# Kernel optimization log

Measured on AMD Instinct MI355X. Metric: run time of the kernel, lower is better.

The kernel has to match this reference:

```python
import jax, jax.numpy as jnp
import numpy as np

NEG = -9e15  # matches torch's -9000000000000000.0 mask value
LN_EPS = 1e-5


def gat_layer(x, adj, W, a, gamma, beta):
    # x: [M, N, Fin], adj: [M, N, N]
    h = x @ W                                  # [M, N, H]
    H = W.shape[1]
    # a([h_i, h_j]) decomposes: e_ij = leakyrelu(h_i.a1 + h_j.a2)
    s_i = h @ a[:H]                            # [M, N]
    s_j = h @ a[H:]                            # [M, N]
    e = jax.nn.leaky_relu(s_i[:, :, None] + s_j[:, None, :], 0.2)
    e = jnp.where(adj > 0, e, NEG)
    att = jax.nn.softmax(e, axis=2)
    hp = jnp.einsum('mij,mjh->mih', att, h)    # bmm aggregation
    mu = hp.mean(-1, keepdims=True)
    var = hp.var(-1, keepdims=True)
    hn = (hp - mu) * jax.lax.rsqrt(var + LN_EPS) * gamma + beta
    return jax.nn.elu(hn)


def lstm_dir(x_seq, Wih, Whh, bih, bhh):
    # x_seq: [B, T, D]; Wih: [D, 4H]; Whh: [H, 4H]; gate order i,f,g,o (torch)
    B = x_seq.shape[0]
    H = Whh.shape[0]
    xg = jnp.einsum('btd,dk->btk', x_seq, Wih) + bih + bhh  # precompute input gates

    def step(carry, xg_t):
        h, c = carry
        g = xg_t + h @ Whh
        i, f, gg, o = jnp.split(g, 4, axis=-1)
        c = jax.nn.sigmoid(f) * c + jax.nn.sigmoid(i) * jnp.tanh(gg)
        h = jax.nn.sigmoid(o) * jnp.tanh(c)
        return (h, c), h

    init = (jnp.zeros((B, H), x_seq.dtype), jnp.zeros((B, H), x_seq.dtype))
    (h_last, _), hs = jax.lax.scan(step, init, jnp.swapaxes(xg, 0, 1))
    return jnp.swapaxes(hs, 0, 1), h_last


def bilstm_layer(x_seq, Wih, Whh, bih, bhh):
    of, hf = lstm_dir(x_seq, Wih[0], Whh[0], bih[0], bhh[0])
    ob, hb = lstm_dir(x_seq[:, ::-1], Wih[1], Whh[1], bih[1], bhh[1])
    return jnp.concatenate([of, ob[:, ::-1]], axis=-1), hf, hb


def setup_inputs() -> dict:
    key = jax.random.key(0)
    ks = jax.random.split(key, 20)
    B, S, N, F, H = 4, 64, 256, 32, 64

    def rn(k, shape, fan_in):
        return jax.random.normal(k, shape, jnp.float32) / np.float32(np.sqrt(fan_in))

    return {
        'x': jax.random.normal(ks[0], (B, S, N, F), jnp.float32),
        'adj': jax.random.randint(ks[1], (B, S, N, N), 0, 2).astype(jnp.float32),
        'gat0_W': rn(ks[2], (F, H), F),
        'gat0_a': rn(ks[3], (2 * H,), 2 * H),
        'gat0_g': jnp.ones((H,), jnp.float32),
        'gat0_b': jnp.zeros((H,), jnp.float32),
        'gat1_W': rn(ks[4], (H, H), H),
        'gat1_a': rn(ks[5], (2 * H,), 2 * H),
        'gat1_g': jnp.ones((H,), jnp.float32),
        'gat1_b': jnp.zeros((H,), jnp.float32),
        'res_W': rn(ks[6], (F, H), F),
        'res_b': jnp.zeros((H,), jnp.float32),
        'alpha_gate': jnp.asarray(0.01, jnp.float32),
        'l0_Wih': rn(ks[7], (2, H, 4 * H), H),
        'l0_Whh': rn(ks[8], (2, H, 4 * H), H),
        'l0_bih': rn(ks[9], (2, 4 * H), H),
        'l0_bhh': rn(ks[10], (2, 4 * H), H),
        'l1_Wih': rn(ks[11], (2, 2 * H, 4 * H), 2 * H),
        'l1_Whh': rn(ks[12], (2, H, 4 * H), H),
        'l1_bih': rn(ks[13], (2, 4 * H), H),
        'l1_bhh': rn(ks[14], (2, 4 * H), H),
        'fc_W': rn(ks[15], (2 * H, 1), 2 * H),
        'fc_b': jnp.zeros((1,), jnp.float32),
    }


def reference(x, adj, gat0_W, gat0_a, gat0_g, gat0_b, gat1_W, gat1_a, gat1_g, gat1_b,
              res_W, res_b, alpha_gate, l0_Wih, l0_Whh, l0_bih, l0_bhh,
              l1_Wih, l1_Whh, l1_bih, l1_bhh, fc_W, fc_b):
    B, S, N, F = x.shape
    x_flat = x.reshape(B * S, N, F)
    adj_flat = adj.reshape(B * S, N, N)

    g = gat_layer(x_flat, adj_flat, gat0_W, gat0_a, gat0_g, gat0_b)
    g = gat_layer(g, adj_flat, gat1_W, gat1_a, gat1_g, gat1_b)

    res = x_flat @ res_W + res_b
    gate = jnp.clip(alpha_gate, 0.0, 1.0)
    comb = res + gate * g                       # [B*S, N, H]
    Hd = comb.shape[-1]

    # [B,S,N,H] -> [B,N,S,H] -> [B*N, S, H]
    seq = comb.reshape(B, S, N, Hd).transpose(0, 2, 1, 3).reshape(B * N, S, Hd)

    o1, _, _ = bilstm_layer(seq, l0_Wih, l0_Whh, l0_bih, l0_bhh)
    _, hf, hb = bilstm_layer(o1, l1_Wih, l1_Whh, l1_bih, l1_bhh)

    final = jnp.concatenate([hf, hb], axis=-1)  # h_n[-2], h_n[-1]
    pred = final @ fc_W + fc_b
    return pred.reshape(B, N, 1)
```

## Files before the change

### kernel.cpp

```cpp
#include <hip/hip_runtime.h>
#include <math.h>

#define BB 4
#define SS 64
#define NN 256
#define FF 32
#define HH 64
#define MM (BB*SS)
#define NSEQ (BB*NN)
#define TT SS
#define MROWS (NSEQ*TT)

__device__ __forceinline__ float fast_rcp(float x) { return __builtin_amdgcn_rcpf(x); }
__device__ __forceinline__ float sigmoid_f(float x) { return fast_rcp(1.0f + __expf(-x)); }
__device__ __forceinline__ float tanh_f(float x) {
    float t = __expf(-2.0f * fabsf(x));
    float r = (1.0f - t) * fast_rcp(1.0f + t);
    return copysignf(r, x);
}

__device__ __forceinline__ void lds_barrier() {
    asm volatile("s_waitcnt lgkmcnt(0)" ::: "memory");
    __builtin_amdgcn_s_barrier();
    __builtin_amdgcn_sched_barrier(0);
}

typedef __bf16 bf16x8 __attribute__((ext_vector_type(8)));
typedef float  f32x4  __attribute__((ext_vector_type(4)));

__device__ __forceinline__ __bf16 bfh(float x) {
    unsigned u = __float_as_uint(x);
    unsigned r = (u + 0x7FFFu + ((u >> 16) & 1u)) >> 16;
    return __builtin_bit_cast(__bf16, (unsigned short)r);
}
__device__ __forceinline__ float bf2f(__bf16 b) {
    unsigned u = ((unsigned)__builtin_bit_cast(unsigned short, b)) << 16;
    return __uint_as_float(u);
}

template<int FIN>
__global__ __launch_bounds__(256) void gat_kernel(
    const float* __restrict__ xin,
    const float* __restrict__ adj,
    const float* __restrict__ W,
    const float* __restrict__ a,
    const float* __restrict__ gamma_, const float* __restrict__ beta_,
    float* __restrict__ gout)
{
    __shared__ __align__(16) float u_f32[256 * 68];
    __shared__ __align__(16) __bf16 p_hi[256 * 40];
    __shared__ __align__(16) __bf16 p_lo[256 * 40];
    __shared__ float s1s[256], s2s[256], srow[256];

    __bf16* F_hi = (__bf16*)u_f32;
    __bf16* F_lo = F_hi + 64 * 264;

    const int m    = blockIdx.x;
    const int tid  = threadIdx.x;
    const int lane = tid & 63;
    const int wv   = tid >> 6;
    const int nl   = lane & 15;
    const int lq   = lane >> 4;

    {
        const int c = tid & 63;
        const int w = tid >> 6;
        float wreg[FIN];
#pragma unroll
        for (int f = 0; f < FIN; ++f) wreg[f] = W[f * 64 + c];
        const float* xm = xin + (size_t)m * NN * FIN;
        for (int i0 = 0; i0 < 64; ++i0) {
            int i = (i0 << 2) | w;
            float acc = 0.0f;
#pragma unroll
            for (int f4 = 0; f4 < FIN / 4; ++f4) {
                float4 xv = *(const float4*)&xm[i * FIN + f4 * 4];
                acc += xv.x * wreg[f4*4] + xv.y * wreg[f4*4+1]
                     + xv.z * wreg[f4*4+2] + xv.w * wreg[f4*4+3];
            }
            u_f32[i * 68 + c] = acc;
        }
    }
    __syncthreads();

    float hr[64];
    {
        const float* hp = &u_f32[tid * 68];
        float acc1 = 0.0f, acc2 = 0.0f;
#pragma unroll
        for (int c4 = 0; c4 < 16; ++c4) {
            float4 hv = *(const float4*)&hp[c4 * 4];
            hr[c4*4+0] = hv.x; hr[c4*4+1] = hv.y; hr[c4*4+2] = hv.z; hr[c4*4+3] = hv.w;
            float4 av1 = *(const float4*)&a[c4 * 4];
            float4 av2 = *(const float4*)&a[64 + c4 * 4];
            acc1 += hv.x * av1.x + hv.y * av1.y + hv.z * av1.z + hv.w * av1.w;
            acc2 += hv.x * av2.x + hv.y * av2.y + hv.z * av2.z + hv.w * av2.w;
        }
        s1s[tid] = acc1; s2s[tid] = acc2;
    }
    __syncthreads();
    {
#pragma unroll
        for (int c = 0; c < 64; ++c) {
            __bf16 hh = bfh(hr[c]);
            F_hi[c * 264 + tid] = hh;
            F_lo[c * 264 + tid] = bfh(hr[c] - bf2f(hh));
        }
    }

    const float* adjr = adj + ((size_t)m * NN + tid) * NN;
    const float s1v = s1s[tid];
    float srow_acc = 0.0f;

    f32x4 acc[4][4];
#pragma unroll
    for (int mt = 0; mt < 4; ++mt)
#pragma unroll
        for (int nt = 0; nt < 4; ++nt)
            acc[mt][nt] = (f32x4){0.0f, 0.0f, 0.0f, 0.0f};

    float4 adjreg[8];
#pragma unroll
    for (int q = 0; q < 8; ++q) adjreg[q] = *(const float4*)&adjr[q * 4];

    for (int ch = 0; ch < 8; ++ch) {
        {
            float pv[32];
#pragma unroll
            for (int q = 0; q < 8; ++q) {
                float4 av = adjreg[q];
                float4 sv = *(const float4*)&s2s[ch * 32 + q * 4];
                float e0 = s1v + sv.x, e1 = s1v + sv.y, e2 = s1v + sv.z, e3 = s1v + sv.w;
                e0 = (e0 > 0.0f) ? e0 : 0.2f * e0;
                e1 = (e1 > 0.0f) ? e1 : 0.2f * e1;
                e2 = (e2 > 0.0f) ? e2 : 0.2f * e2;
                e3 = (e3 > 0.0f) ? e3 : 0.2f * e3;
                float p0 = (av.x > 0.0f) ? __expf(e0) : 0.0f;
                float p1 = (av.y > 0.0f) ? __expf(e1) : 0.0f;
                float p2 = (av.z > 0.0f) ? __expf(e2) : 0.0f;
                float p3 = (av.w > 0.0f) ? __expf(e3) : 0.0f;
                srow_acc += (p0 + p1) + (p2 + p3);
                pv[q*4+0] = p0; pv[q*4+1] = p1; pv[q*4+2] = p2; pv[q*4+3] = p3;
            }
#pragma unroll
            for (int b = 0; b < 4; ++b) {
                bf16x8 h8, l8;
#pragma unroll
                for (int j = 0; j < 8; ++j) {
                    __bf16 hh = bfh(pv[b*8+j]);
                    h8[j] = hh;
                    l8[j] = bfh(pv[b*8+j] - bf2f(hh));
                }
                *(bf16x8*)&p_hi[tid * 40 + b * 8] = h8;
                *(bf16x8*)&p_lo[tid * 40 + b * 8] = l8;
            }
        }
        if (ch < 7) {
#pragma unroll
            for (int q = 0; q < 8; ++q)
                adjreg[q] = *(const float4*)&adjr[(ch + 1) * 32 + q * 4];
        }
        lds_barrier();

        bf16x8 pah[4], pal[4], fbh[4], fbl[4];
#pragma unroll
        for (int mt = 0; mt < 4; ++mt) {
            int row = wv * 64 + mt * 16 + nl;
            pah[mt] = *(const bf16x8*)&p_hi[row * 40 + lq * 8];
            pal[mt] = *(const bf16x8*)&p_lo[row * 40 + lq * 8];
        }
#pragma unroll
        for (int nt = 0; nt < 4; ++nt) {
            int fo = (nt * 16 + nl) * 264 + ch * 32 + lq * 8;
            fbh[nt] = *(const bf16x8*)&F_hi[fo];
            fbl[nt] = *(const bf16x8*)&F_lo[fo];
        }
#pragma unroll
        for (int mt = 0; mt < 4; ++mt)
#pragma unroll
            for (int nt = 0; nt < 4; ++nt)
                acc[mt][nt] = __builtin_amdgcn_mfma_f32_16x16x32_bf16(
                    pah[mt], fbh[nt], acc[mt][nt], 0, 0, 0);
#pragma unroll
        for (int mt = 0; mt < 4; ++mt)
#pragma unroll
            for (int nt = 0; nt < 4; ++nt)
                acc[mt][nt] = __builtin_amdgcn_mfma_f32_16x16x32_bf16(
                    pal[mt], fbh[nt], acc[mt][nt], 0, 0, 0);
#pragma unroll
        for (int mt = 0; mt < 4; ++mt)
#pragma unroll
            for (int nt = 0; nt < 4; ++nt)
                acc[mt][nt] = __builtin_amdgcn_mfma_f32_16x16x32_bf16(
                    pah[mt], fbl[nt], acc[mt][nt], 0, 0, 0);

        lds_barrier();
    }

    srow[tid] = srow_acc;
    __syncthreads();

    float gm[4], bt[4];
#pragma unroll
    for (int nt = 0; nt < 4; ++nt) {
        gm[nt] = gamma_[nt * 16 + nl];
        bt[nt] = beta_[nt * 16 + nl];
    }
#pragma unroll
    for (int mt = 0; mt < 4; ++mt) {
#pragma unroll
        for (int r = 0; r < 4; ++r) {
            int row = wv * 64 + mt * 16 + lq * 4 + r;
            float rinv = fast_rcp(srow[row]);
            float v[4];
            float sm = 0.0f, sq = 0.0f;
#pragma unroll
            for (int nt = 0; nt < 4; ++nt) {
                v[nt] = acc[mt][nt][r] * rinv;
                sm += v[nt]; sq += v[nt] * v[nt];
            }
#pragma unroll
            for (int off = 1; off < 16; off <<= 1) {
                sm += __shfl_xor(sm, off);
                sq += __shfl_xor(sq, off);
            }
            float mu  = sm * (1.0f / 64.0f);
            float var = sq * (1.0f / 64.0f) - mu * mu;
            float rs  = rsqrtf(var + 1e-5f);
            float* gp = &gout[((size_t)m * NN + row) * 64];
#pragma unroll
            for (int nt = 0; nt < 4; ++nt) {
                float hn = (v[nt] - mu) * rs * gm[nt] + bt[nt];
                gp[nt * 16 + nl] = (hn > 0.0f) ? hn : (__expf(hn) - 1.0f);
            }
        }
    }
}

__global__ __launch_bounds__(256) void combine_kernel(
    const float* __restrict__ x,
    const float* __restrict__ g1,
    const float* __restrict__ res_W,
    const float* __restrict__ res_b,
    const float* __restrict__ alpha_p,
    float* __restrict__ seqout)
{
    int row = blockIdx.x * 4 + (threadIdx.x >> 6);
    int h = threadIdx.x & 63;
    int mg = row >> 8, n = row & 255;
    int b = mg >> 6, s = mg & 63;
    const float* xr = x + (size_t)row * 32;
    float acc = res_b[h];
#pragma unroll
    for (int f4 = 0; f4 < 8; ++f4) {
        float4 xv = *(const float4*)&xr[f4 * 4];
        acc += xv.x * res_W[(f4*4    ) * 64 + h] + xv.y * res_W[(f4*4 + 1) * 64 + h]
             + xv.z * res_W[(f4*4 + 2) * 64 + h] + xv.w * res_W[(f4*4 + 3) * 64 + h];
    }
    float alpha = fminf(fmaxf(alpha_p[0], 0.0f), 1.0f);
    acc += alpha * g1[(size_t)row * 64 + h];
    seqout[(((size_t)(b * NN + n)) * TT + s) * 64 + h] = acc;
}

template<int K>
__global__ __launch_bounds__(256) void wcvt_kernel(
    const float* __restrict__ Wih, __bf16* __restrict__ Wh, __bf16* __restrict__ Wl)
{
    constexpr int NKC = K / 32;
    int idx = blockIdx.x * 256 + threadIdx.x;
    int j   = idx & 7;
    int nl  = (idx >> 3) & 15;
    int g   = (idx >> 7) & 3;
    int ng  = (idx >> 9) & 15;
    int rest = idx >> 13;
    int kc  = rest & (NKC - 1);
    int dir = rest / NKC;
    int k = kc * 32 + g * 8 + j;
    int n = ng * 16 + nl;
    float x = Wih[((size_t)dir * K + k) * 256 + n];
    __bf16 h = bfh(x);
    Wh[idx] = h;
    Wl[idx] = bfh(x - bf2f(h));
}

__global__ __launch_bounds__(256) void whhcvt_kernel(
    const float* __restrict__ W0, const float* __restrict__ W1,
    __bf16* __restrict__ outw)
{
    int idx = blockIdx.x * 256 + threadIdx.x;
    int lay = idx >> 15;
    int r   = idx & 32767;
    int j   = r & 7;
    int nl  = (r >> 3) & 15;
    int g   = (r >> 7) & 3;
    int ng  = (r >> 9) & 15;
    int rest = r >> 13;
    int kc  = rest & 1;
    int dir = rest >> 1;
    int k = kc * 32 + g * 8 + j;
    int n = ng * 16 + nl;
    const float* W = lay ? W1 : W0;
    float x = W[((size_t)dir * 64 + k) * 256 + n];
    __bf16 h = bfh(x);
    outw[lay * 65536 + r]         = h;
    outw[lay * 65536 + 32768 + r] = bfh(x - bf2f(h));
}

template<int K>
__global__ __launch_bounds__(256, 2) void xg_mfma_kernel(
    const float* __restrict__ A,
    const __bf16* __restrict__ Wh,
    const __bf16* __restrict__ Wl,
    const float* __restrict__ bih,
    const float* __restrict__ bhh,
    float* __restrict__ xg)
{
    constexpr int NKC = K / 32;
    __shared__ __bf16 a_h[2][128 * 32];
    __shared__ __bf16 a_l[2][128 * 32];

    const int tid  = threadIdx.x;
    const int lane = tid & 63;
    const int w    = tid >> 6;
    const int wr   = w >> 1, wc = w & 1;

    int bid = blockIdx.x;
    int wg  = (bid >> 3) | ((bid & 7) << 8);
    int cd  = wg & 3;
    int m0  = (wg >> 2) * 128;
    int dir = cd >> 1;
    const int kq = (cd & 1) * 2 + wc;

    f32x4 acc[4][4];
#pragma unroll
    for (int mi = 0; mi < 4; ++mi)
#pragma unroll
        for (int ni = 0; ni < 4; ++ni)
            acc[mi][ni] = (f32x4){0.0f, 0.0f, 0.0f, 0.0f};

    const int srow = tid >> 1;
    const int g0   = (tid & 1) * 2;
    const float* abase = A + (size_t)(m0 + srow) * K + (tid & 1) * 16;
    const int soff0 = srow * 32 + (( g0      ^ (srow & 3)) * 8);
    const int soff1 = srow * 32 + (((g0 + 1) ^ (srow & 3)) * 8);

    int aoff[4];
#pragma unroll
    for (int mi = 0; mi < 4; ++mi)
        aoff[mi] = (wr * 64 + mi * 16 + (lane & 15)) * 32
                 + (((lane >> 4) ^ (lane & 3)) * 8);

    auto cvtstore = [&](const float* f, int buf) {
        bf16x8 h0, h1, l0, l1;
#pragma unroll
        for (int i = 0; i < 8; ++i) {
            __bf16 ha = bfh(f[i]);
            __bf16 hb = bfh(f[8 + i]);
            h0[i] = ha; l0[i] = bfh(f[i]     - bf2f(ha));
            h1[i] = hb; l1[i] = bfh(f[8 + i] - bf2f(hb));
        }
        *(bf16x8*)&a_h[buf][soff0] = h0;
        *(bf16x8*)&a_h[buf][soff1] = h1;
        *(bf16x8*)&a_l[buf][soff0] = l0;
        *(bf16x8*)&a_l[buf][soff1] = l1;
    };

    {
        float f[16];
#pragma unroll
        for (int i = 0; i < 4; ++i) {
            float4 v = *(const float4*)(abase + i * 4);
            f[i*4+0] = v.x; f[i*4+1] = v.y; f[i*4+2] = v.z; f[i*4+3] = v.w;
        }
        cvtstore(f, 0);
    }
    lds_barrier();

    int buf = 0;
    for (int kc = 0; kc < NKC; ++kc) {
        float f[16];
        if (kc + 1 < NKC) {
#pragma unroll
            for (int i = 0; i < 4; ++i) {
                float4 v = *(const float4*)(abase + (kc + 1) * 32 + i * 4);
                f[i*4+0] = v.x; f[i*4+1] = v.y; f[i*4+2] = v.z; f[i*4+3] = v.w;
            }
        }
        bf16x8 bh[4], bl[4];
#pragma unroll
        for (int ni = 0; ni < 4; ++ni) {
            size_t fb = ((size_t)((dir * NKC + kc) * 16 + ni * 4 + kq)) * 512 + lane * 8;
            bh[ni] = *(const bf16x8*)(Wh + fb);
            bl[ni] = *(const bf16x8*)(Wl + fb);
        }
        bf16x8 ah[4], al[4];
#pragma unroll
        for (int mi = 0; mi < 4; ++mi) {
            ah[mi] = *(const bf16x8*)&a_h[buf][aoff[mi]];
            al[mi] = *(const bf16x8*)&a_l[buf][aoff[mi]];
        }
#pragma unroll
        for (int mi = 0; mi < 4; ++mi)
#pragma unroll
            for (int ni = 0; ni < 4; ++ni)
                acc[mi][ni] = __builtin_amdgcn_mfma_f32_16x16x32_bf16(
                    ah[mi], bh[ni], acc[mi][ni], 0, 0, 0);
#pragma unroll
        for (int mi = 0; mi < 4; ++mi)
#pragma unroll
            for (int ni = 0; ni < 4; ++ni)
                acc[mi][ni] = __builtin_amdgcn_mfma_f32_16x16x32_bf16(
                    al[mi], bh[ni], acc[mi][ni], 0, 0, 0);
#pragma unroll
        for (int mi = 0; mi < 4; ++mi)
#pragma unroll
            for (int ni = 0; ni < 4; ++ni)
                acc[mi][ni] = __builtin_amdgcn_mfma_f32_16x16x32_bf16(
                    ah[mi], bl[ni], acc[mi][ni], 0, 0, 0);

        if (kc + 1 < NKC) cvtstore(f, buf ^ 1);
        lds_barrier();
        buf ^= 1;
    }

    const int kcol = kq * 16 + (lane & 15);
    float bias4[4];
#pragma unroll
    for (int g = 0; g < 4; ++g)
        bias4[g] = bih[dir * 256 + g * 64 + kcol] + bhh[dir * 256 + g * 64 + kcol];
#pragma unroll
    for (int mi = 0; mi < 4; ++mi) {
        int mrow = m0 + wr * 64 + mi * 16 + ((lane >> 4) << 2);
#pragma unroll
        for (int r = 0; r < 4; ++r) {
            float4 v = make_float4(acc[mi][0][r] + bias4[0], acc[mi][1][r] + bias4[1],
                                   acc[mi][2][r] + bias4[2], acc[mi][3][r] + bias4[3]);
            *(float4*)&xg[((size_t)dir * MROWS + mrow + r) * 256 + kcol * 4] = v;
        }
    }
}

__global__ __launch_bounds__(256, 2) void lstm_rec_kernel(
    const float* __restrict__ xg,
    const __bf16* __restrict__ whhf,
    float* __restrict__ out,
    int write_all)
{
    const int tid  = threadIdx.x;
    const int wv   = tid >> 6;
    const int lane = tid & 63;
    const int nl   = lane & 15;
    const int lq   = lane >> 4;

    const int bid  = blockIdx.x;
    const int dir  = bid & 1;
    const int seq0 = (bid >> 1) * 4;

    const __bf16* wh = whhf;
    const __bf16* wl = whhf + 32768;
    bf16x8 bh[2][4], bl[2][4];
#pragma unroll
    for (int kc = 0; kc < 2; ++kc)
#pragma unroll
        for (int g = 0; g < 4; ++g) {
            size_t fb = ((size_t)((dir * 2 + kc) * 16 + g * 4 + wv)) * 512 + lane * 8;
            bh[kc][g] = *(const bf16x8*)(wh + fb);
            bl[kc][g] = *(const bf16x8*)(wl + fb);
        }

    __shared__ __align__(16) __bf16 h_hi[2048];
    __shared__ __align__(16) __bf16 h_lo[2048];
    {
        uint4 z = {0, 0, 0, 0};
        *(uint4*)&h_hi[tid * 8] = z;
        *(uint4*)&h_lo[tid * 8] = z;
    }

    const int k   = wv * 16 + nl;
    const int g8k = k >> 3;

    float c = 0.0f;
    float4 xa = {}, xb = {};

    const float* pxg = xg + (((size_t)dir * NSEQ + seq0 + lq) * TT
                             + (dir ? (TT - 1) : 0)) * 256 + k * 4;
    const int dstep = dir ? -256 : 256;
    float* pout = out + (((size_t)(seq0 + lq)) * TT + (dir ? (TT - 1) : 0)) * 128
                + dir * 64 + k;
    const int ostep = dir ? -128 : 128;

    auto load_xg = [&](float4& d) {
        d = *(const float4*)pxg;
        pxg += dstep;
    };

    int buf = 0;
    auto step_body = [&](int step, float4& xcur, float4& xnext, bool pre) {
        const int aof0 = buf * 1024 + nl * 64 + (((0 + lq) ^ (nl & 7)) * 8);
        const int aof1 = buf * 1024 + nl * 64 + (((4 + lq) ^ (nl & 7)) * 8);
        bf16x8 ah0 = *(const bf16x8*)&h_hi[aof0];
        bf16x8 ah1 = *(const bf16x8*)&h_hi[aof1];
        bf16x8 al0 = *(const bf16x8*)&h_lo[aof0];
        bf16x8 al1 = *(const bf16x8*)&h_lo[aof1];

        if (pre) load_xg(xnext);

        f32x4 acc[4];
#pragma unroll
        for (int g = 0; g < 4; ++g) acc[g] = (f32x4){0.0f, 0.0f, 0.0f, 0.0f};
#pragma unroll
        for (int g = 0; g < 4; ++g)
            acc[g] = __builtin_amdgcn_mfma_f32_16x16x32_bf16(ah0, bh[0][g], acc[g], 0, 0, 0);
#pragma unroll
        for (int g = 0; g < 4; ++g)
            acc[g] = __builtin_amdgcn_mfma_f32_16x16x32_bf16(ah1, bh[1][g], acc[g], 0, 0, 0);
#pragma unroll
        for (int g = 0; g < 4; ++g)
            acc[g] = __builtin_amdgcn_mfma_f32_16x16x32_bf16(al0, bh[0][g], acc[g], 0, 0, 0);
#pragma unroll
        for (int g = 0; g < 4; ++g)
            acc[g] = __builtin_amdgcn_mfma_f32_16x16x32_bf16(al1, bh[1][g], acc[g], 0, 0, 0);
#pragma unroll
        for (int g = 0; g < 4; ++g)
            acc[g] = __builtin_amdgcn_mfma_f32_16x16x32_bf16(ah0, bl[0][g], acc[g], 0, 0, 0);
#pragma unroll
        for (int g = 0; g < 4; ++g)
            acc[g] = __builtin_amdgcn_mfma_f32_16x16x32_bf16(ah1, bl[1][g], acc[g], 0, 0, 0);

        float pre4[4];
#pragma unroll
        for (int g = 0; g < 4; ++g) {
            float b0 = __shfl(acc[g][0], nl);
            float b1 = __shfl(acc[g][1], nl);
            float b2 = __shfl(acc[g][2], nl);
            float b3 = __shfl(acc[g][3], nl);
            float v01 = (lq & 1) ? b1 : b0;
            float v23 = (lq & 1) ? b3 : b2;
            pre4[g] = (lq & 2) ? v23 : v01;
        }

        float iv = sigmoid_f(pre4[0] + xcur.x);
        float fv = sigmoid_f(pre4[1] + xcur.y);
        float gv = tanh_f  (pre4[2] + xcur.z);
        float ov = sigmoid_f(pre4[3] + xcur.w);
        c = fv * c + iv * gv;
        float h = ov * tanh_f(c);
        int off = (buf ^ 1) * 1024 + lq * 64 + ((g8k ^ lq) * 8) + (k & 7);
        __bf16 hh = bfh(h);
        h_hi[off] = hh;
        h_lo[off] = bfh(h - bf2f(hh));
        if (write_all)
            pout[0] = h;
        else if (step == TT - 1)
            out[(size_t)(seq0 + lq) * 128 + dir * 64 + k] = h;
        pout += ostep;
        lds_barrier();
        buf ^= 1;
    };

    load_xg(xa);
    lds_barrier();

    for (int step = 0; step < TT; step += 2) {
        step_body(step,     xa, xb, true);
        step_body(step + 1, xb, xa, step + 2 < TT);
    }
}

__global__ __launch_bounds__(256) void fc_kernel(
    const float* __restrict__ fin,
    const float* __restrict__ fc_W,
    const float* __restrict__ fc_b,
    float* __restrict__ outp)
{
    int s = blockIdx.x * 256 + threadIdx.x;
    const float* fr = fin + (size_t)s * 128;
    float acc = fc_b[0];
#pragma unroll
    for (int k4 = 0; k4 < 32; ++k4) {
        float4 fv = *(const float4*)&fr[k4 * 4];
        float4 wv2 = *(const float4*)&fc_W[k4 * 4];
        acc += fv.x * wv2.x + fv.y * wv2.y + fv.z * wv2.z + fv.w * wv2.w;
    }
    outp[s] = acc;
}

extern "C" void kernel_launch(void* const* d_in, const int* in_sizes, int n_in,
                              void* d_out, int out_size, void* d_ws, size_t ws_size,
                              hipStream_t stream) {
    const float* x       = (const float*)d_in[0];
    const float* adj     = (const float*)d_in[1];
    const float* gat0_W  = (const float*)d_in[2];
    const float* gat0_a  = (const float*)d_in[3];
    const float* gat0_g  = (const float*)d_in[4];
    const float* gat0_b  = (const float*)d_in[5];
    const float* gat1_W  = (const float*)d_in[6];
    const float* gat1_a  = (const float*)d_in[7];
    const float* gat1_g  = (const float*)d_in[8];
    const float* gat1_b  = (const float*)d_in[9];
    const float* res_W   = (const float*)d_in[10];
    const float* res_b   = (const float*)d_in[11];
    const float* alpha_g = (const float*)d_in[12];
    const float* l0_Wih  = (const float*)d_in[13];
    const float* l0_Whh  = (const float*)d_in[14];
    const float* l0_bih  = (const float*)d_in[15];
    const float* l0_bhh  = (const float*)d_in[16];
    const float* l1_Wih  = (const float*)d_in[17];
    const float* l1_Whh  = (const float*)d_in[18];
    const float* l1_bih  = (const float*)d_in[19];
    const float* l1_bhh  = (const float*)d_in[20];
    const float* fc_W    = (const float*)d_in[21];
    const float* fc_b    = (const float*)d_in[22];

    float* ws = (float*)d_ws;
    float* g0    = ws;
    float* g1    = ws + 4194304;
    float* seq   = ws + 8388608;
    float* xg    = ws + 12582912;
    float* fin   = ws + 46137344;
    float* o1    = ws;

    __bf16* w0h = (__bf16*)(ws + 46137344);
    __bf16* w0l = w0h + 2 * 64 * 256;
    __bf16* w1h = w0l + 2 * 64 * 256;
    __bf16* w1l = w1h + 2 * 128 * 256;

    __bf16* whhf = (__bf16*)seq;

    wcvt_kernel<64><<<128, 256, 0, stream>>>(l0_Wih, w0h, w0l);
    wcvt_kernel<128><<<256, 256, 0, stream>>>(l1_Wih, w1h, w1l);
    gat_kernel<32><<<MM, 256, 0, stream>>>(x, adj, gat0_W, gat0_a, gat0_g, gat0_b, g0);
    gat_kernel<64><<<MM, 256, 0, stream>>>(g0, adj, gat1_W, gat1_a, gat1_g, gat1_b, g1);
    combine_kernel<<<(BB*SS*NN)/4, 256, 0, stream>>>(x, g1, res_W, res_b, alpha_g, seq);
    xg_mfma_kernel<64><<<2048, 256, 0, stream>>>(seq, w0h, w0l, l0_bih, l0_bhh, xg);
    whhcvt_kernel<<<256, 256, 0, stream>>>(l0_Whh, l1_Whh, whhf);
    lstm_rec_kernel<<<512, 256, 0, stream>>>(xg, whhf, o1, 1);
    xg_mfma_kernel<128><<<2048, 256, 0, stream>>>(o1, w1h, w1l, l1_bih, l1_bhh, xg);
    lstm_rec_kernel<<<512, 256, 0, stream>>>(xg, whhf + 65536, fin, 0);
    fc_kernel<<<NSEQ/256, 256, 0, stream>>>(fin, fc_W, fc_b, (float*)d_out);
}
```

Measured before the change: 470.6 us.

## Use 512 threads per GAT block, splitting each node row across two threads

The GAT kernel now runs 512 threads per block. Each node row is handled by a pair of threads that split the feature columns and adjacency columns, with shuffle reductions for the attention scores and row sums. Each wave now covers 32 rows instead of 64 in the MFMA aggregation. The aim is to hide more latency with more waves and to lower per-thread register pressure (hr, adjreg, acc). In exchange there are extra shuffles and barriers that span more waves.

```diff
diff --git a/kernel.cpp b/kernel.cpp
--- a/kernel.cpp
+++ b/kernel.cpp
@@ -39,7 +39,7 @@
 }
 
 template<int FIN>
-__global__ __launch_bounds__(256) void gat_kernel(
+__global__ __launch_bounds__(512) void gat_kernel(
     const float* __restrict__ xin,
     const float* __restrict__ adj,
     const float* __restrict__ W,
@@ -61,16 +61,17 @@
     const int wv   = tid >> 6;
     const int nl   = lane & 15;
     const int lq   = lane >> 4;
+    const int row2 = tid >> 1;
+    const int half = tid & 1;
 
     {
         const int c = tid & 63;
-        const int w = tid >> 6;
         float wreg[FIN];
 #pragma unroll
         for (int f = 0; f < FIN; ++f) wreg[f] = W[f * 64 + c];
         const float* xm = xin + (size_t)m * NN * FIN;
-        for (int i0 = 0; i0 < 64; ++i0) {
-            int i = (i0 << 2) | w;
+        for (int i0 = 0; i0 < 32; ++i0) {
+            int i = (i0 << 3) | wv;
             float acc = 0.0f;
 #pragma unroll
             for (int f4 = 0; f4 < FIN / 4; ++f4) {
@@ -83,53 +84,56 @@
     }
     __syncthreads();
 
-    float hr[64];
+    float hr[32];
     {
-        const float* hp = &u_f32[tid * 68];
+        const float* hp = &u_f32[row2 * 68 + half * 32];
         float acc1 = 0.0f, acc2 = 0.0f;
 #pragma unroll
-        for (int c4 = 0; c4 < 16; ++c4) {
+        for (int c4 = 0; c4 < 8; ++c4) {
             float4 hv = *(const float4*)&hp[c4 * 4];
             hr[c4*4+0] = hv.x; hr[c4*4+1] = hv.y; hr[c4*4+2] = hv.z; hr[c4*4+3] = hv.w;
-            float4 av1 = *(const float4*)&a[c4 * 4];
-            float4 av2 = *(const float4*)&a[64 + c4 * 4];
+            float4 av1 = *(const float4*)&a[half * 32 + c4 * 4];
+            float4 av2 = *(const float4*)&a[64 + half * 32 + c4 * 4];
             acc1 += hv.x * av1.x + hv.y * av1.y + hv.z * av1.z + hv.w * av1.w;
             acc2 += hv.x * av2.x + hv.y * av2.y + hv.z * av2.z + hv.w * av2.w;
         }
-        s1s[tid] = acc1; s2s[tid] = acc2;
+        acc1 += __shfl_xor(acc1, 1);
+        acc2 += __shfl_xor(acc2, 1);
+        if (half == 0) { s1s[row2] = acc1; s2s[row2] = acc2; }
     }
     __syncthreads();
     {
 #pragma unroll
-        for (int c = 0; c < 64; ++c) {
-            __bf16 hh = bfh(hr[c]);
-            F_hi[c * 264 + tid] = hh;
-            F_lo[c * 264 + tid] = bfh(hr[c] - bf2f(hh));
-        }
-    }
-
-    const float* adjr = adj + ((size_t)m * NN + tid) * NN;
-    const float s1v = s1s[tid];
+        for (int cc = 0; cc < 32; ++cc) {
+            int c = half * 32 + cc;
+            __bf16 hh = bfh(hr[cc]);
+            F_hi[c * 264 + row2] = hh;
+            F_lo[c * 264 + row2] = bfh(hr[cc] - bf2f(hh));
+        }
+    }
+
+    const float* adjr = adj + ((size_t)m * NN + row2) * NN + half * 16;
+    const float s1v = s1s[row2];
     float srow_acc = 0.0f;
 
-    f32x4 acc[4][4];
-#pragma unroll
-    for (int mt = 0; mt < 4; ++mt)
+    f32x4 acc[2][4];
+#pragma unroll
+    for (int mt = 0; mt < 2; ++mt)
 #pragma unroll
         for (int nt = 0; nt < 4; ++nt)
             acc[mt][nt] = (f32x4){0.0f, 0.0f, 0.0f, 0.0f};
 
-    float4 adjreg[8];
-#pragma unroll
-    for (int q = 0; q < 8; ++q) adjreg[q] = *(const float4*)&adjr[q * 4];
+    float4 adjreg[4];
+#pragma unroll
+    for (int q = 0; q < 4; ++q) adjreg[q] = *(const float4*)&adjr[q * 4];
 
     for (int ch = 0; ch < 8; ++ch) {
         {
-            float pv[32];
-#pragma unroll
-            for (int q = 0; q < 8; ++q) {
+            float pv[16];
+#pragma unroll
+            for (int q = 0; q < 4; ++q) {
                 float4 av = adjreg[q];
-                float4 sv = *(const float4*)&s2s[ch * 32 + q * 4];
+                float4 sv = *(const float4*)&s2s[ch * 32 + half * 16 + q * 4];
                 float e0 = s1v + sv.x, e1 = s1v + sv.y, e2 = s1v + sv.z, e3 = s1v + sv.w;
                 e0 = (e0 > 0.0f) ? e0 : 0.2f * e0;
                 e1 = (e1 > 0.0f) ? e1 : 0.2f * e1;
@@ -143,7 +147,7 @@
                 pv[q*4+0] = p0; pv[q*4+1] = p1; pv[q*4+2] = p2; pv[q*4+3] = p3;
             }
 #pragma unroll
-            for (int b = 0; b < 4; ++b) {
+            for (int b = 0; b < 2; ++b) {
                 bf16x8 h8, l8;
 #pragma unroll
                 for (int j = 0; j < 8; ++j) {
@@ -151,21 +155,21 @@
                     h8[j] = hh;
                     l8[j] = bfh(pv[b*8+j] - bf2f(hh));
                 }
-                *(bf16x8*)&p_hi[tid * 40 + b * 8] = h8;
-                *(bf16x8*)&p_lo[tid * 40 + b * 8] = l8;
+                *(bf16x8*)&p_hi[row2 * 40 + half * 16 + b * 8] = h8;
+                *(bf16x8*)&p_lo[row2 * 40 + half * 16 + b * 8] = l8;
             }
         }
         if (ch < 7) {
 #pragma unroll
-            for (int q = 0; q < 8; ++q)
+            for (int q = 0; q < 4; ++q)
                 adjreg[q] = *(const float4*)&adjr[(ch + 1) * 32 + q * 4];
         }
         lds_barrier();
 
-        bf16x8 pah[4], pal[4], fbh[4], fbl[4];
-#pragma unroll
-        for (int mt = 0; mt < 4; ++mt) {
-            int row = wv * 64 + mt * 16 + nl;
+        bf16x8 pah[2], pal[2], fbh[4], fbl[4];
+#pragma unroll
+        for (int mt = 0; mt < 2; ++mt) {
+            int row = wv * 32 + mt * 16 + nl;
             pah[mt] = *(const bf16x8*)&p_hi[row * 40 + lq * 8];
             pal[mt] = *(const bf16x8*)&p_lo[row * 40 + lq * 8];
         }
@@ -176,19 +180,19 @@
             fbl[nt] = *(const bf16x8*)&F_lo[fo];
         }
 #pragma unroll
-        for (int mt = 0; mt < 4; ++mt)
+        for (int mt = 0; mt < 2; ++mt)
 #pragma unroll
             for (int nt = 0; nt < 4; ++nt)
                 acc[mt][nt] = __builtin_amdgcn_mfma_f32_16x16x32_bf16(
                     pah[mt], fbh[nt], acc[mt][nt], 0, 0, 0);
 #pragma unroll
-        for (int mt = 0; mt < 4; ++mt)
+        for (int mt = 0; mt < 2; ++mt)
 #pragma unroll
             for (int nt = 0; nt < 4; ++nt)
                 acc[mt][nt] = __builtin_amdgcn_mfma_f32_16x16x32_bf16(
                     pal[mt], fbh[nt], acc[mt][nt], 0, 0, 0);
 #pragma unroll
-        for (int mt = 0; mt < 4; ++mt)
+        for (int mt = 0; mt < 2; ++mt)
 #pragma unroll
             for (int nt = 0; nt < 4; ++nt)
                 acc[mt][nt] = __builtin_amdgcn_mfma_f32_16x16x32_bf16(
@@ -197,7 +201,10 @@
         lds_barrier();
     }
 
-    srow[tid] = srow_acc;
+    {
+        float sr = srow_acc + __shfl_xor(srow_acc, 1);
+        if (half == 0) srow[row2] = sr;
+    }
     __syncthreads();
 
     float gm[4], bt[4];
@@ -207,10 +214,10 @@
         bt[nt] = beta_[nt * 16 + nl];
     }
 #pragma unroll
-    for (int mt = 0; mt < 4; ++mt) {
+    for (int mt = 0; mt < 2; ++mt) {
 #pragma unroll
         for (int r = 0; r < 4; ++r) {
-            int row = wv * 64 + mt * 16 + lq * 4 + r;
+            int row = wv * 32 + mt * 16 + lq * 4 + r;
             float rinv = fast_rcp(srow[row]);
             float v[4];
             float sm = 0.0f, sq = 0.0f;
@@ -629,8 +636,8 @@
 
     wcvt_kernel<64><<<128, 256, 0, stream>>>(l0_Wih, w0h, w0l);
     wcvt_kernel<128><<<256, 256, 0, stream>>>(l1_Wih, w1h, w1l);
-    gat_kernel<32><<<MM, 256, 0, stream>>>(x, adj, gat0_W, gat0_a, gat0_g, gat0_b, g0);
-    gat_kernel<64><<<MM, 256, 0, stream>>>(g0, adj, gat1_W, gat1_a, gat1_g, gat1_b, g1);
+    gat_kernel<32><<<MM, 512, 0, stream>>>(x, adj, gat0_W, gat0_a, gat0_g, gat0_b, g0);
+    gat_kernel<64><<<MM, 512, 0, stream>>>(g0, adj, gat1_W, gat1_a, gat1_g, gat1_b, g1);
     combine_kernel<<<(BB*SS*NN)/4, 256, 0, stream>>>(x, g1, res_W, res_b, alpha_g, seq);
     xg_mfma_kernel<64><<<2048, 256, 0, stream>>>(seq, w0h, w0l, l0_bih, l0_bhh, xg);
     whhcvt_kernel<<<256, 256, 0, stream>>>(l0_Whh, l1_Whh, whhf);
```

Result: faster. 442.7 us (-5.9%).
